# Optimization experiments

Hardware: AMD Instinct MI355X
Metric: run time of the kernel (lower is better)

The kernel has to match this reference:

```python
import jax, jax.numpy as jnp
import numpy as np

N_NODES = 10000
N_EDGES = 160000
H = 128          # n_hidden_feat
K1 = 64          # n_Gaussian
K2 = 64          # n_grid_K**3
NB = 3           # N_block
G = 100          # number of graphs in batch
CUTOFF = 8.0


def setup_inputs() -> dict:
    key = jax.random.key(0)
    ks = jax.random.split(key, 20)
    s = 0.05
    return {
        'x': jax.random.normal(ks[0], (N_NODES, H), jnp.float32),
        'edge_distance': jax.random.uniform(ks[1], (N_EDGES,), jnp.float32, 0.5, 10.0),
        'combine_sets': jax.random.normal(ks[2], (N_EDGES, K1), jnp.float32),
        'plane_wave': jax.random.normal(ks[3], (N_EDGES, K2), jnp.float32),
        'emb_W': jax.random.normal(ks[4], (H, H), jnp.float32) * s,
        'conv_Wgate': jax.random.normal(ks[5], (NB, 3 * H, H), jnp.float32) * s,
        'conv_Wmlp': jax.random.normal(ks[6], (NB, 3 * H, H), jnp.float32) * s,
        'conv_W1': jax.random.normal(ks[7], (NB, K1, H), jnp.float32) * s,
        'conv_W2g': jax.random.normal(ks[8], (NB, K2, K2), jnp.float32) * s,
        'conv_W2': jax.random.normal(ks[9], (NB, K2, H), jnp.float32) * s,
        'pool_W1': jax.random.normal(ks[10], (NB, H, H), jnp.float32) * s,
        'pool_W2': jax.random.normal(ks[11], (NB, H, H), jnp.float32) * s,
        'psi_W': jax.random.normal(ks[12], (NB, H, H), jnp.float32) * s,
        'lr_W1': jax.random.normal(ks[13], (H, H // 2), jnp.float32) * s,
        'lr_W2': jax.random.normal(ks[14], (H // 2, H // 4), jnp.float32) * s,
        'edge_sources': jax.random.randint(ks[15], (N_EDGES,), 0, N_NODES, jnp.int32),
        'edge_targets': jax.random.randint(ks[16], (N_EDGES,), 0, N_NODES, jnp.int32),
        'graph_indices': jnp.sort(jax.random.randint(ks[17], (N_NODES,), 0, G, jnp.int32)),
        'node_counts': jax.random.randint(ks[18], (G,), 1, 200, jnp.int32),
    }


def reference(x, edge_distance, combine_sets, plane_wave, emb_W,
              conv_Wgate, conv_Wmlp, conv_W1, conv_W2g, conv_W2,
              pool_W1, pool_W2, psi_W, lr_W1, lr_W2,
              edge_sources, edge_targets, graph_indices, node_counts):
    n_graphs = node_counts.shape[0]
    elu = jax.nn.elu
    sig = jax.nn.sigmoid

    # NodeEmbedding (sigmoid activation, no bias)
    h = sig(x @ emb_W)                                   # [N, H]

    r = edge_distance[:, None]                           # [E, 1]
    mask = (r < CUTOFF).astype(h.dtype)                  # [E, 1]

    pooled_sum = jnp.zeros((n_graphs, h.shape[1]), h.dtype)
    for i in range(conv_Wgate.shape[0]):                 # N_block (small fixed)
        # --- GatedGraphConvolution ---
        ni = h[edge_sources]                             # [E, H] gather
        nj = h[edge_targets]                             # [E, H] gather
        fe = jnp.concatenate([ni, nj, (ni - nj) / r], axis=1)  # [E, 3H]
        e_gate = sig(fe @ conv_Wgate[i])                 # [E, H]
        e_mlp = elu(fe @ conv_Wmlp[i])                   # [E, H]
        z1 = combine_sets @ conv_W1[i]                   # [E, H]
        pw_gate = sig(plane_wave @ conv_W2g[i])          # [E, K2]
        z2 = (plane_wave * pw_gate) @ conv_W2[i]         # [E, H]
        z = e_gate * e_mlp * (z1 + z2) * mask            # [E, H]
        h = h.at[edge_sources].add(z)                    # scatter-add (index_add_)
        # --- Gated_pooling (note: original discards /node_counts -> sum pool) ---
        zp = elu((h @ pool_W1[i]) * (h @ pool_W2[i]))    # [N, H]
        pooled_sum = pooled_sum + jax.ops.segment_sum(zp, graph_indices, num_segments=n_graphs)
        # --- MLP_psi2n ---
        h = elu(h @ psi_W[i])

    y = elu(pooled_sum @ lr_W1)                          # [G, H/2]
    y = elu(y @ lr_W2)                                   # [G, H/4]
    return y
```

## Files before the change

### kernel.cpp

```cpp
#include <hip/hip_runtime.h>
#include <math.h>

#define H 128
#define N_NODES 10000
#define N_EDGES 160000

typedef float f32x4 __attribute__((ext_vector_type(4)));
typedef short s16x8 __attribute__((ext_vector_type(8)));

#define WAVE_LDS_FENCE() do { \
  asm volatile("s_waitcnt lgkmcnt(0)" ::: "memory"); \
  __builtin_amdgcn_sched_barrier(0); \
} while (0)

__device__ __forceinline__ float sigf(float x){ return 1.0f/(1.0f + __expf(-x)); }
__device__ __forceinline__ float eluf(float x){ return x > 0.0f ? x : (__expf(x) - 1.0f); }

__device__ __forceinline__ unsigned short f2bf(float f){
  unsigned int u = __float_as_uint(f);
  unsigned int r = (u + 0x7fffu + ((u >> 16) & 1u)) >> 16;
  return (unsigned short)r;
}
__device__ __forceinline__ float bf2f(unsigned short s){
  return __uint_as_float(((unsigned int)s) << 16);
}

__device__ __forceinline__ f32x4 MFMA16(s16x8 a, s16x8 b, f32x4 c){
  return __builtin_amdgcn_mfma_f32_16x16x32_bf16(a, b, c, 0, 0, 0);
}

__device__ __forceinline__ s16x8 loadA_f32(const float* p){
  float4 a = *(const float4*)p;
  float4 b = *(const float4*)(p+4);
  s16x8 r;
  r[0]=(short)f2bf(a.x); r[1]=(short)f2bf(a.y); r[2]=(short)f2bf(a.z); r[3]=(short)f2bf(a.w);
  r[4]=(short)f2bf(b.x); r[5]=(short)f2bf(b.y); r[6]=(short)f2bf(b.z); r[7]=(short)f2bf(b.w);
  return r;
}

__global__ __launch_bounds__(256) void hist_kernel(
    const int* __restrict__ src, const float* __restrict__ ed, int* __restrict__ count)
{
  int e = blockIdx.x*256 + threadIdx.x;
  if (e < N_EDGES && ed[e] < 8.0f) atomicAdd(&count[src[e]], 1);
}

__global__ __launch_bounds__(256) void scan_kernel(
    const int* __restrict__ count, int* __restrict__ offsets)
{
  __shared__ int tmp[256];
  __shared__ int sbase;
  if (threadIdx.x == 0) sbase = 0;
  __syncthreads();
  for (int c0 = 0; c0 < N_NODES; c0 += 256) {
    int i = c0 + threadIdx.x;
    int v = (i < N_NODES) ? count[i] : 0;
    tmp[threadIdx.x] = v;
    __syncthreads();
    for (int off = 1; off < 256; off <<= 1) {
      int t = (threadIdx.x >= off) ? tmp[threadIdx.x - off] : 0;
      __syncthreads();
      tmp[threadIdx.x] += t;
      __syncthreads();
    }
    if (i < N_NODES) offsets[i] = sbase + tmp[threadIdx.x] - v;
    __syncthreads();
    if (threadIdx.x == 255) sbase += tmp[255];
    __syncthreads();
  }
  if (threadIdx.x == 0) offsets[N_NODES] = sbase;
}

__global__ __launch_bounds__(256) void scatter_kernel(
    const int* __restrict__ src, const int* __restrict__ tgt, const float* __restrict__ ed,
    const int* __restrict__ offsets,
    int* __restrict__ cursor, int* __restrict__ mcur, int* __restrict__ perm,
    int* __restrict__ srcp, int* __restrict__ tgtp, float* __restrict__ edp)
{
  int e = blockIdx.x*256 + threadIdx.x;
  if (e < N_EDGES) {
    int s = src[e];
    float r = ed[e];
    int pos;
    if (r < 8.0f) pos = atomicAdd(&cursor[s], 1);
    else          pos = offsets[N_NODES] + atomicAdd(mcur, 1);
    perm[pos] = e;
    srcp[pos] = s;
    tgtp[pos] = tgt[e];
    edp[pos]  = r;
  }
}

__global__ __launch_bounds__(256) void prep_edges(
    const float* __restrict__ cs, const float* __restrict__ pw, const int* __restrict__ perm,
    unsigned short* __restrict__ csb, unsigned short* __restrict__ pwb)
{
  int idx = blockIdx.x*256 + threadIdx.x;
  if (idx >= N_EDGES*8) return;
  int pos = idx >> 3, kc = idx & 7;
  int e = perm[pos];
  s16x8 c = loadA_f32(&cs[(size_t)e*64 + kc*8]);
  s16x8 p = loadA_f32(&pw[(size_t)e*64 + kc*8]);
  *(s16x8*)&csb[(size_t)pos*64 + kc*8] = c;
  *(s16x8*)&pwb[(size_t)pos*64 + kc*8] = p;
}

__global__ __launch_bounds__(256) void prep_weights(
    const float* __restrict__ W1, const float* __restrict__ W2, const float* __restrict__ W2g,
    const float* __restrict__ embW,
    unsigned short* __restrict__ w1t, unsigned short* __restrict__ w2t,
    unsigned short* __restrict__ w2gt, unsigned short* __restrict__ embt)
{
  int idx = blockIdx.x*256 + threadIdx.x;
  if (idx < 3*8192) {
    int l = idx / 8192, r = idx % 8192;
    int c = r >> 6, k = r & 63;
    w1t[idx] = f2bf(W1[l*8192 + k*128 + c]);
    w2t[idx] = f2bf(W2[l*8192 + k*128 + c]);
  } else if (idx < 3*8192 + 3*4096) {
    int idx2 = idx - 3*8192;
    int l = idx2 / 4096, r = idx2 % 4096;
    int c = r >> 6, k = r & 63;
    w2gt[idx2] = f2bf(W2g[l*4096 + k*64 + c]);
  } else {
    int idx3 = idx - (3*8192 + 3*4096);
    if (idx3 < 16384) {
      int c = idx3 >> 7, k = idx3 & 127;
      embt[idx3] = f2bf(embW[k*128 + c]);
    }
  }
}

__global__ __launch_bounds__(256) void prep_nodew(
    const float* __restrict__ Wg, const float* __restrict__ Wm,
    const float* __restrict__ p1, const float* __restrict__ p2, const float* __restrict__ psiW,
    unsigned short* __restrict__ wnt, unsigned short* __restrict__ wpt)
{
  int idx = blockIdx.x*256 + threadIdx.x;
  if (idx < 3*98304) {
    int l = idx / 98304, r = idx % 98304;
    int j = r >> 7, k = r & 127;
    float v;
    if (j < 384) v = Wg[l*49152 + (j>>7)*16384 + k*128 + (j&127)];
    else { int jj = j - 384; v = Wm[l*49152 + (jj>>7)*16384 + k*128 + (jj&127)]; }
    wnt[idx] = f2bf(v);
  } else {
    int idx2 = idx - 3*98304;
    if (idx2 < 3*49152) {
      int l = idx2 / 49152, r = idx2 % 49152;
      int j = r >> 7, k = r & 127;
      float v;
      if (j < 128)      v = p1 [l*16384 + k*128 + j];
      else if (j < 256) v = p2 [l*16384 + k*128 + (j-128)];
      else              v = psiW[l*16384 + k*128 + (j-256)];
      wpt[idx2] = f2bf(v);
    }
  }
}

__global__ __launch_bounds__(256) void embed_pack(
    const float* __restrict__ x, const unsigned short* __restrict__ embt,
    const unsigned short* __restrict__ wnt,
    float* __restrict__ h_out,
    unsigned short* __restrict__ spackb, unsigned short* __restrict__ tpackb)
{
  __shared__ unsigned short hb[16*128];
  int tid = threadIdx.x, wave = tid >> 6, lane = tid & 63;
  int row = lane & 15, kg = lane >> 4;
  int nbase = blockIdx.x*16;
  const float* xr = &x[(size_t)(nbase + row)*H];
  s16x8 a[4];
  #pragma unroll
  for (int ks = 0; ks < 4; ks++) a[ks] = loadA_f32(xr + ks*32 + kg*8);

  f32x4 acc[2];
  #pragma unroll
  for (int ti = 0; ti < 2; ti++) { acc[ti][0]=0.f; acc[ti][1]=0.f; acc[ti][2]=0.f; acc[ti][3]=0.f; }
  #pragma unroll
  for (int ti = 0; ti < 2; ti++) {
    int col = (wave*2 + ti)*16 + row;
    #pragma unroll
    for (int ks = 0; ks < 4; ks++) {
      s16x8 b = *(const s16x8*)&embt[(size_t)col*128 + ks*32 + kg*8];
      acc[ti] = MFMA16(a[ks], b, acc[ti]);
    }
  }
  #pragma unroll
  for (int ti = 0; ti < 2; ti++) {
    int col = (wave*2 + ti)*16 + row;
    #pragma unroll
    for (int r = 0; r < 4; r++) {
      int ln = kg*4 + r;
      float v = sigf(acc[ti][r]);
      h_out[(size_t)(nbase + ln)*H + col] = v;
      int byt = (ln << 8) + (col << 1);
      byt ^= (ln & 7) << 4;
      *(unsigned short*)((char*)hb + byt) = f2bf(v);
    }
  }
  __syncthreads();

  s16x8 an[4];
  #pragma unroll
  for (int ks = 0; ks < 4; ks++) {
    int byt = (row << 8) + ks*64 + kg*16;
    byt ^= (row & 7) << 4;
    an[ks] = *(s16x8*)((char*)hb + byt);
  }
  #pragma unroll
  for (int ti = 0; ti < 2; ti++) {
    int t = wave*2 + ti;
    f32x4 pacc[6];
    #pragma unroll
    for (int ch = 0; ch < 6; ch++) { pacc[ch][0]=0.f; pacc[ch][1]=0.f; pacc[ch][2]=0.f; pacc[ch][3]=0.f; }
    #pragma unroll
    for (int ch = 0; ch < 6; ch++) {
      int col = ch*128 + t*16 + row;
      #pragma unroll
      for (int ks = 0; ks < 4; ks++) {
        s16x8 b = *(const s16x8*)&wnt[(size_t)col*128 + ks*32 + kg*8];
        pacc[ch] = MFMA16(an[ks], b, pacc[ch]);
      }
    }
    int c = t*16 + row;
    #pragma unroll
    for (int r = 0; r < 4; r++) {
      int nc = nbase + kg*4 + r;
      size_t base = (size_t)nc*512 + c*4;
      unsigned int s0 = (unsigned int)f2bf(pacc[0][r]) | ((unsigned int)f2bf(pacc[2][r]) << 16);
      unsigned int s1 = (unsigned int)f2bf(pacc[3][r]) | ((unsigned int)f2bf(pacc[5][r]) << 16);
      unsigned int t0 = (unsigned int)f2bf(pacc[1][r]) | ((unsigned int)f2bf(pacc[2][r]) << 16);
      unsigned int t1 = (unsigned int)f2bf(pacc[4][r]) | ((unsigned int)f2bf(pacc[5][r]) << 16);
      *(uint2*)&spackb[base] = make_uint2(s0, s1);
      *(uint2*)&tpackb[base] = make_uint2(t0, t1);
    }
  }
}

__global__ __launch_bounds__(256) void fused_edge(
    float* __restrict__ h_acc,
    const unsigned short* __restrict__ csb, const unsigned short* __restrict__ pwb,
    const unsigned short* __restrict__ w1t, const unsigned short* __restrict__ w2t,
    const unsigned short* __restrict__ w2gt,
    const int* __restrict__ srcp, const int* __restrict__ tgtp,
    const float* __restrict__ edp, const int* __restrict__ nact,
    const unsigned short* __restrict__ spackb, const unsigned short* __restrict__ tpackb)
{
  __shared__ unsigned short zb[4][16][132];
  __shared__ int   src_s[4][16];
  __shared__ int   tgt_s[4][16];
  __shared__ float rcp_s[4][16];
  __shared__ float msk_s[4][16];

  int p0 = blockIdx.x * 64;
  if (p0 >= *nact) return;

  int tid  = threadIdx.x;
  int wave = tid >> 6, lane = tid & 63;
  int row  = lane & 15, kg = lane >> 4;
  unsigned short* gate = &zb[wave][0][0];

  if (lane < 16) {
    int e = p0 + wave*16 + lane;
    float r = edp[e];
    rcp_s[wave][lane] = 1.0f / r;
    msk_s[wave][lane] = (r < 8.0f) ? 1.0f : 0.0f;
    src_s[wave][lane] = srcp[e];
    tgt_s[wave][lane] = tgtp[e];
  }

  int pos = p0 + wave*16 + row;
  s16x8 acs[2], apw[2];
  acs[0] = *(const s16x8*)&csb[(size_t)pos*64 + kg*8];
  acs[1] = *(const s16x8*)&csb[(size_t)pos*64 + 32 + kg*8];
  apw[0] = *(const s16x8*)&pwb[(size_t)pos*64 + kg*8];
  apw[1] = *(const s16x8*)&pwb[(size_t)pos*64 + 32 + kg*8];

  f32x4 acc1[4];
  #pragma unroll
  for (int nt = 0; nt < 4; nt++) { acc1[nt][0]=0.f; acc1[nt][1]=0.f; acc1[nt][2]=0.f; acc1[nt][3]=0.f; }
  #pragma unroll
  for (int nt = 0; nt < 4; nt++) {
    s16x8 b0 = *(const s16x8*)&w2gt[(size_t)(nt*16+row)*64 + kg*8];
    s16x8 b1 = *(const s16x8*)&w2gt[(size_t)(nt*16+row)*64 + 32 + kg*8];
    acc1[nt] = MFMA16(apw[0], b0, acc1[nt]);
    acc1[nt] = MFMA16(apw[1], b1, acc1[nt]);
  }

  #pragma unroll
  for (int nt = 0; nt < 4; nt++) {
    #pragma unroll
    for (int r = 0; r < 4; r++) {
      int grow = kg*4 + r;
      int gcol = nt*16 + row;
      int byt = (grow << 7) + (gcol << 1);
      byt ^= (grow & 7) << 4;
      *(unsigned short*)((char*)gate + byt) = f2bf(sigf(acc1[nt][r]));
    }
  }
  WAVE_LDS_FENCE();

  s16x8 apg[2];
  #pragma unroll
  for (int ks = 0; ks < 2; ks++) {
    int byt = (row << 7) + ks*64 + kg*16;
    byt ^= (row & 7) << 4;
    s16x8 g = *(s16x8*)((char*)gate + byt);
    s16x8 o;
    #pragma unroll
    for (int j = 0; j < 8; j++) {
      float v = bf2f((unsigned short)apw[ks][j]) * bf2f((unsigned short)g[j]);
      o[j] = (short)f2bf(v);
    }
    apg[ks] = o;
  }
  WAVE_LDS_FENCE();

  f32x4 acc2[8];
  #pragma unroll
  for (int nt = 0; nt < 8; nt++) { acc2[nt][0]=0.f; acc2[nt][1]=0.f; acc2[nt][2]=0.f; acc2[nt][3]=0.f; }
  #pragma unroll
  for (int nt = 0; nt < 8; nt++) {
    #pragma unroll
    for (int ks = 0; ks < 2; ks++) {
      s16x8 b1 = *(const s16x8*)&w1t[(size_t)(nt*16+row)*64 + ks*32 + kg*8];
      acc2[nt] = MFMA16(acs[ks], b1, acc2[nt]);
      s16x8 b2 = *(const s16x8*)&w2t[(size_t)(nt*16+row)*64 + ks*32 + kg*8];
      acc2[nt] = MFMA16(apg[ks], b2, acc2[nt]);
    }
  }

  #pragma unroll
  for (int nt = 0; nt < 8; nt++) {
    #pragma unroll
    for (int r = 0; r < 4; r++) {
      zb[wave][kg*4 + r][nt*16 + row] = f2bf(acc2[nt][r]);
    }
  }
  WAVE_LDS_FENCE();

  {
    int l = lane;
    int cur = src_s[wave][0];
    s16x8 sp = *(const s16x8*)&spackb[(size_t)cur*512 + l*8];
    float Ags0 = bf2f((unsigned short)sp[0]), Cgs0 = bf2f((unsigned short)sp[1]);
    float Ams0 = bf2f((unsigned short)sp[2]), Cms0 = bf2f((unsigned short)sp[3]);
    float Ags1 = bf2f((unsigned short)sp[4]), Cgs1 = bf2f((unsigned short)sp[5]);
    float Ams1 = bf2f((unsigned short)sp[6]), Cms1 = bf2f((unsigned short)sp[7]);
    float acc0 = 0.f, accB = 0.f;
    for (int eb = 0; eb < 16; eb += 4) {
      s16x8 tp[4]; unsigned int zz[4];
      #pragma unroll
      for (int b = 0; b < 4; b++) {
        int e = eb + b;
        tp[b] = *(const s16x8*)&tpackb[(size_t)tgt_s[wave][e]*512 + l*8];
        zz[b] = *(const unsigned int*)&zb[wave][e][2*l];
      }
      #pragma unroll
      for (int b = 0; b < 4; b++) {
        int e = eb + b;
        int sn = src_s[wave][e];
        if (sn != cur) {
          atomicAdd(&h_acc[(size_t)cur*H + 2*l],     acc0);
          atomicAdd(&h_acc[(size_t)cur*H + 2*l + 1], accB);
          acc0 = 0.f; accB = 0.f; cur = sn;
          sp = *(const s16x8*)&spackb[(size_t)cur*512 + l*8];
          Ags0 = bf2f((unsigned short)sp[0]); Cgs0 = bf2f((unsigned short)sp[1]);
          Ams0 = bf2f((unsigned short)sp[2]); Cms0 = bf2f((unsigned short)sp[3]);
          Ags1 = bf2f((unsigned short)sp[4]); Cgs1 = bf2f((unsigned short)sp[5]);
          Ams1 = bf2f((unsigned short)sp[6]); Cms1 = bf2f((unsigned short)sp[7]);
        }
        float rc = rcp_s[wave][e], mk = msk_s[wave][e];
        float z0 = bf2f((unsigned short)(zz[b] & 0xffffu));
        float z1 = bf2f((unsigned short)(zz[b] >> 16));
        float Bg0 = bf2f((unsigned short)tp[b][0]), Cg0 = bf2f((unsigned short)tp[b][1]);
        float Bm0 = bf2f((unsigned short)tp[b][2]), Cm0 = bf2f((unsigned short)tp[b][3]);
        float Bg1 = bf2f((unsigned short)tp[b][4]), Cg1 = bf2f((unsigned short)tp[b][5]);
        float Bm1 = bf2f((unsigned short)tp[b][6]), Cm1 = bf2f((unsigned short)tp[b][7]);
        float g0 = sigf(Ags0 + Bg0 + rc*(Cgs0 - Cg0));
        float m0 = eluf(Ams0 + Bm0 + rc*(Cms0 - Cm0));
        acc0 += g0 * m0 * z0 * mk;
        float g1 = sigf(Ags1 + Bg1 + rc*(Cgs1 - Cg1));
        float m1 = eluf(Ams1 + Bm1 + rc*(Cms1 - Cm1));
        accB += g1 * m1 * z1 * mk;
      }
    }
    atomicAdd(&h_acc[(size_t)cur*H + 2*l],     acc0);
    atomicAdd(&h_acc[(size_t)cur*H + 2*l + 1], accB);
  }
}

__global__ __launch_bounds__(256) void node_next(
    float* __restrict__ h,
    const unsigned short* __restrict__ wpt,
    const unsigned short* __restrict__ wnt,
    const int* __restrict__ gidx, float* __restrict__ pooled,
    unsigned short* __restrict__ spackb, unsigned short* __restrict__ tpackb,
    int has_next)
{
  __shared__ unsigned short hb[16*128];
  int tid = threadIdx.x, wave = tid >> 6, lane = tid & 63;
  int row = lane & 15, kg = lane >> 4;
  int nbase = blockIdx.x*16;
  const float* hr = &h[(size_t)(nbase + row)*H];
  s16x8 a[4];
  #pragma unroll
  for (int ks = 0; ks < 4; ks++) a[ks] = loadA_f32(hr + ks*32 + kg*8);

  f32x4 acc1[2], acc2[2], acc3[2];
  #pragma unroll
  for (int ti = 0; ti < 2; ti++) {
    #pragma unroll
    for (int r = 0; r < 4; r++) { acc1[ti][r]=0.f; acc2[ti][r]=0.f; acc3[ti][r]=0.f; }
  }
  #pragma unroll
  for (int ti = 0; ti < 2; ti++) {
    int col = (wave*2 + ti)*16 + row;
    #pragma unroll
    for (int ks = 0; ks < 4; ks++) {
      s16x8 b1 = *(const s16x8*)&wpt[(size_t)(col      )*128 + ks*32 + kg*8];
      s16x8 b2 = *(const s16x8*)&wpt[(size_t)(col + 128)*128 + ks*32 + kg*8];
      s16x8 b3 = *(const s16x8*)&wpt[(size_t)(col + 256)*128 + ks*32 + kg*8];
      acc1[ti] = MFMA16(a[ks], b1, acc1[ti]);
      acc2[ti] = MFMA16(a[ks], b2, acc2[ti]);
      acc3[ti] = MFMA16(a[ks], b3, acc3[ti]);
    }
  }

  int nc0 = nbase + kg*4;
  int g0 = gidx[nc0], g3 = gidx[nc0 + 3];
  if (g0 == g3) {
    #pragma unroll
    for (int ti = 0; ti < 2; ti++) {
      int col = (wave*2 + ti)*16 + row;
      float s = 0.f;
      #pragma unroll
      for (int r = 0; r < 4; r++) s += eluf(acc1[ti][r] * acc2[ti][r]);
      atomicAdd(&pooled[g0*H + col], s);
      #pragma unroll
      for (int r = 0; r < 4; r++) {
        int ln = kg*4 + r;
        float v = eluf(acc3[ti][r]);
        h[(size_t)(nc0 + r)*H + col] = v;
        int byt = (ln << 8) + (col << 1);
        byt ^= (ln & 7) << 4;
        *(unsigned short*)((char*)hb + byt) = f2bf(v);
      }
    }
  } else {
    #pragma unroll
    for (int r = 0; r < 4; r++) {
      int nc = nc0 + r;
      int ln = kg*4 + r;
      int g = gidx[nc];
      #pragma unroll
      for (int ti = 0; ti < 2; ti++) {
        int col = (wave*2 + ti)*16 + row;
        float zp = eluf(acc1[ti][r] * acc2[ti][r]);
        atomicAdd(&pooled[g*H + col], zp);
        float v = eluf(acc3[ti][r]);
        h[(size_t)nc*H + col] = v;
        int byt = (ln << 8) + (col << 1);
        byt ^= (ln & 7) << 4;
        *(unsigned short*)((char*)hb + byt) = f2bf(v);
      }
    }
  }
  if (!has_next) return;
  __syncthreads();

  s16x8 an[4];
  #pragma unroll
  for (int ks = 0; ks < 4; ks++) {
    int byt = (row << 8) + ks*64 + kg*16;
    byt ^= (row & 7) << 4;
    an[ks] = *(s16x8*)((char*)hb + byt);
  }
  #pragma unroll
  for (int ti = 0; ti < 2; ti++) {
    int t = wave*2 + ti;
    f32x4 pacc[6];
    #pragma unroll
    for (int ch = 0; ch < 6; ch++) { pacc[ch][0]=0.f; pacc[ch][1]=0.f; pacc[ch][2]=0.f; pacc[ch][3]=0.f; }
    #pragma unroll
    for (int ch = 0; ch < 6; ch++) {
      int col = ch*128 + t*16 + row;
      #pragma unroll
      for (int ks = 0; ks < 4; ks++) {
        s16x8 b = *(const s16x8*)&wnt[(size_t)col*128 + ks*32 + kg*8];
        pacc[ch] = MFMA16(an[ks], b, pacc[ch]);
      }
    }
    int c = t*16 + row;
    #pragma unroll
    for (int r = 0; r < 4; r++) {
      int nc = nbase + kg*4 + r;
      size_t base = (size_t)nc*512 + c*4;
      unsigned int s0 = (unsigned int)f2bf(pacc[0][r]) | ((unsigned int)f2bf(pacc[2][r]) << 16);
      unsigned int s1 = (unsigned int)f2bf(pacc[3][r]) | ((unsigned int)f2bf(pacc[5][r]) << 16);
      unsigned int t0 = (unsigned int)f2bf(pacc[1][r]) | ((unsigned int)f2bf(pacc[2][r]) << 16);
      unsigned int t1 = (unsigned int)f2bf(pacc[4][r]) | ((unsigned int)f2bf(pacc[5][r]) << 16);
      *(uint2*)&spackb[base] = make_uint2(s0, s1);
      *(uint2*)&tpackb[base] = make_uint2(t0, t1);
    }
  }
}

__global__ __launch_bounds__(64) void final_kernel(
    const float* __restrict__ pooled, const float* __restrict__ lr1, const float* __restrict__ lr2,
    float* __restrict__ out)
{
  __shared__ float sp[128];
  __shared__ float y1[64];
  int g = blockIdx.x, tid = threadIdx.x;
  sp[tid]      = pooled[g*128 + tid];
  sp[tid + 64] = pooled[g*128 + 64 + tid];
  __syncthreads();
  float acc = 0.f;
  for (int k = 0; k < 128; k++) acc += sp[k] * lr1[k*64 + tid];
  y1[tid] = eluf(acc);
  __syncthreads();
  if (tid < 32) {
    float a2 = 0.f;
    for (int k = 0; k < 64; k++) a2 += y1[k] * lr2[k*32 + tid];
    out[g*32 + tid] = eluf(a2);
  }
}

extern "C" void kernel_launch(void* const* d_in, const int* in_sizes, int n_in,
                              void* d_out, int out_size, void* d_ws, size_t ws_size,
                              hipStream_t stream)
{
  const float* x    = (const float*)d_in[0];
  const float* ed   = (const float*)d_in[1];
  const float* cs   = (const float*)d_in[2];
  const float* pw   = (const float*)d_in[3];
  const float* embW = (const float*)d_in[4];
  const float* Wg   = (const float*)d_in[5];
  const float* Wm   = (const float*)d_in[6];
  const float* W1   = (const float*)d_in[7];
  const float* W2g  = (const float*)d_in[8];
  const float* W2   = (const float*)d_in[9];
  const float* p1   = (const float*)d_in[10];
  const float* p2   = (const float*)d_in[11];
  const float* psiW = (const float*)d_in[12];
  const float* lr1  = (const float*)d_in[13];
  const float* lr2  = (const float*)d_in[14];
  const int* esrc   = (const int*)d_in[15];
  const int* etgt   = (const int*)d_in[16];
  const int* gidx   = (const int*)d_in[17];

  float* h_b    = (float*)d_ws;
  float* pooled = h_b + (size_t)N_NODES*H;
  unsigned short* spackb = (unsigned short*)(pooled + 100*H);
  unsigned short* tpackb = spackb + (size_t)N_NODES*512;
  int* counts  = (int*)(tpackb + (size_t)N_NODES*512);
  int* offsets = counts + N_NODES;
  int* cursor  = offsets + N_NODES + 1;
  int* mcur    = cursor + N_NODES;
  int* perm    = mcur + 1;
  int* srcp    = perm + N_EDGES;
  int* tgtp    = srcp + N_EDGES;
  float* edp   = (float*)(tgtp + N_EDGES);
  unsigned short* w1t  = (unsigned short*)(edp + N_EDGES);
  unsigned short* w2t  = w1t + 3*8192;
  unsigned short* w2gt = w2t + 3*8192;
  unsigned short* embt = w2gt + 3*4096;
  unsigned short* wnt  = embt + 16384;
  unsigned short* wpt  = wnt + 3*98304;
  unsigned short* csb  = wpt + 3*49152;
  unsigned short* pwb  = csb + (size_t)N_EDGES*64;

  hipMemsetAsync(counts, 0, N_NODES*sizeof(int), stream);
  hipMemsetAsync(mcur, 0, sizeof(int), stream);
  hipMemsetAsync(pooled, 0, 100*H*sizeof(float), stream);
  hist_kernel<<<(N_EDGES+255)/256, 256, 0, stream>>>(esrc, ed, counts);
  scan_kernel<<<1, 256, 0, stream>>>(counts, offsets);
  hipMemcpyAsync(cursor, offsets, N_NODES*sizeof(int), hipMemcpyDeviceToDevice, stream);
  scatter_kernel<<<(N_EDGES+255)/256, 256, 0, stream>>>(esrc, etgt, ed, offsets,
      cursor, mcur, perm, srcp, tgtp, edp);
  prep_edges<<<N_EDGES*8/256, 256, 0, stream>>>(cs, pw, perm, csb, pwb);
  prep_weights<<<208, 256, 0, stream>>>(W1, W2, W2g, embW, w1t, w2t, w2gt, embt);
  prep_nodew<<<(3*98304 + 3*49152 + 255)/256, 256, 0, stream>>>(Wg, Wm, p1, p2, psiW, wnt, wpt);

  embed_pack<<<N_NODES/16, 256, 0, stream>>>(x, embt, wnt, h_b, spackb, tpackb);

  for (int i = 0; i < 3; i++) {
    fused_edge<<<N_EDGES/64, 256, 0, stream>>>(h_b, csb, pwb,
        w1t + i*8192, w2t + i*8192, w2gt + i*4096,
        srcp, tgtp, edp, offsets + N_NODES, spackb, tpackb);
    node_next<<<N_NODES/16, 256, 0, stream>>>(h_b,
        wpt + i*49152, wnt + ((i+1) % 3)*98304,
        gidx, pooled, spackb, tpackb, (i < 2) ? 1 : 0);
  }
  final_kernel<<<100, 64, 0, stream>>>(pooled, lr1, lr2, (float*)d_out);
}
```

Measured before the change: 428.6 us.

## Process 32 edges per wave in fused_edge and widen node_next to 8 waves

fused_edge now handles 128 edges per block, with each wave doing two 16-row sub-tiles, which halves the grid and lengthens each wave's scatter run so fewer atomic flushes happen at segment boundaries. node_next runs with 512 threads, one 16-column tile per wave instead of two, to raise parallelism and cut per-thread register use. prep_edges zero-fills rows past the active edge count and skips their gathers, so the now-padded tiles read defined data and no work is spent on masked edges. The costs are higher LDS and register use per fused_edge block and an extra block-wide barrier in node_next.

Result: slower. 461.4 us (+7.7%).

```diff
diff --git a/kernel.cpp b/kernel.cpp
--- a/kernel.cpp
+++ b/kernel.cpp
@@ -93,16 +93,23 @@
 
 __global__ __launch_bounds__(256) void prep_edges(
     const float* __restrict__ cs, const float* __restrict__ pw, const int* __restrict__ perm,
+    const int* __restrict__ nact,
     unsigned short* __restrict__ csb, unsigned short* __restrict__ pwb)
 {
   int idx = blockIdx.x*256 + threadIdx.x;
   if (idx >= N_EDGES*8) return;
   int pos = idx >> 3, kc = idx & 7;
-  int e = perm[pos];
-  s16x8 c = loadA_f32(&cs[(size_t)e*64 + kc*8]);
-  s16x8 p = loadA_f32(&pw[(size_t)e*64 + kc*8]);
-  *(s16x8*)&csb[(size_t)pos*64 + kc*8] = c;
-  *(s16x8*)&pwb[(size_t)pos*64 + kc*8] = p;
+  if (pos < *nact) {
+    int e = perm[pos];
+    s16x8 c = loadA_f32(&cs[(size_t)e*64 + kc*8]);
+    s16x8 p = loadA_f32(&pw[(size_t)e*64 + kc*8]);
+    *(s16x8*)&csb[(size_t)pos*64 + kc*8] = c;
+    *(s16x8*)&pwb[(size_t)pos*64 + kc*8] = p;
+  } else {
+    s16x8 z = {0,0,0,0,0,0,0,0};
+    *(s16x8*)&csb[(size_t)pos*64 + kc*8] = z;
+    *(s16x8*)&pwb[(size_t)pos*64 + kc*8] = z;
+  }
 }
 
 __global__ __launch_bounds__(256) void prep_weights(
@@ -246,22 +253,21 @@
     const float* __restrict__ edp, const int* __restrict__ nact,
     const unsigned short* __restrict__ spackb, const unsigned short* __restrict__ tpackb)
 {
-  __shared__ unsigned short zb[4][16][132];
-  __shared__ int   src_s[4][16];
-  __shared__ int   tgt_s[4][16];
-  __shared__ float rcp_s[4][16];
-  __shared__ float msk_s[4][16];
-
-  int p0 = blockIdx.x * 64;
+  __shared__ unsigned short zb[4][32][132];
+  __shared__ int   src_s[4][32];
+  __shared__ int   tgt_s[4][32];
+  __shared__ float rcp_s[4][32];
+  __shared__ float msk_s[4][32];
+
+  int p0 = blockIdx.x * 128;
   if (p0 >= *nact) return;
 
   int tid  = threadIdx.x;
   int wave = tid >> 6, lane = tid & 63;
   int row  = lane & 15, kg = lane >> 4;
-  unsigned short* gate = &zb[wave][0][0];
-
-  if (lane < 16) {
-    int e = p0 + wave*16 + lane;
+
+  if (lane < 32) {
+    int e = p0 + wave*32 + lane;
     float r = edp[e];
     rcp_s[wave][lane] = 1.0f / r;
     msk_s[wave][lane] = (r < 8.0f) ? 1.0f : 0.0f;
@@ -269,72 +275,76 @@
     tgt_s[wave][lane] = tgtp[e];
   }
 
-  int pos = p0 + wave*16 + row;
-  s16x8 acs[2], apw[2];
-  acs[0] = *(const s16x8*)&csb[(size_t)pos*64 + kg*8];
-  acs[1] = *(const s16x8*)&csb[(size_t)pos*64 + 32 + kg*8];
-  apw[0] = *(const s16x8*)&pwb[(size_t)pos*64 + kg*8];
-  apw[1] = *(const s16x8*)&pwb[(size_t)pos*64 + 32 + kg*8];
-
-  f32x4 acc1[4];
-  #pragma unroll
-  for (int nt = 0; nt < 4; nt++) { acc1[nt][0]=0.f; acc1[nt][1]=0.f; acc1[nt][2]=0.f; acc1[nt][3]=0.f; }
-  #pragma unroll
-  for (int nt = 0; nt < 4; nt++) {
-    s16x8 b0 = *(const s16x8*)&w2gt[(size_t)(nt*16+row)*64 + kg*8];
-    s16x8 b1 = *(const s16x8*)&w2gt[(size_t)(nt*16+row)*64 + 32 + kg*8];
-    acc1[nt] = MFMA16(apw[0], b0, acc1[nt]);
-    acc1[nt] = MFMA16(apw[1], b1, acc1[nt]);
-  }
-
-  #pragma unroll
-  for (int nt = 0; nt < 4; nt++) {
-    #pragma unroll
-    for (int r = 0; r < 4; r++) {
-      int grow = kg*4 + r;
-      int gcol = nt*16 + row;
-      int byt = (grow << 7) + (gcol << 1);
-      byt ^= (grow & 7) << 4;
-      *(unsigned short*)((char*)gate + byt) = f2bf(sigf(acc1[nt][r]));
-    }
-  }
-  WAVE_LDS_FENCE();
-
-  s16x8 apg[2];
-  #pragma unroll
-  for (int ks = 0; ks < 2; ks++) {
-    int byt = (row << 7) + ks*64 + kg*16;
-    byt ^= (row & 7) << 4;
-    s16x8 g = *(s16x8*)((char*)gate + byt);
-    s16x8 o;
-    #pragma unroll
-    for (int j = 0; j < 8; j++) {
-      float v = bf2f((unsigned short)apw[ks][j]) * bf2f((unsigned short)g[j]);
-      o[j] = (short)f2bf(v);
-    }
-    apg[ks] = o;
-  }
-  WAVE_LDS_FENCE();
-
-  f32x4 acc2[8];
-  #pragma unroll
-  for (int nt = 0; nt < 8; nt++) { acc2[nt][0]=0.f; acc2[nt][1]=0.f; acc2[nt][2]=0.f; acc2[nt][3]=0.f; }
-  #pragma unroll
-  for (int nt = 0; nt < 8; nt++) {
+  #pragma unroll
+  for (int hf2 = 0; hf2 < 2; hf2++) {
+    unsigned short* gate = &zb[wave][hf2*16][0];
+    int pos = p0 + wave*32 + hf2*16 + row;
+    s16x8 acs[2], apw[2];
+    acs[0] = *(const s16x8*)&csb[(size_t)pos*64 + kg*8];
+    acs[1] = *(const s16x8*)&csb[(size_t)pos*64 + 32 + kg*8];
+    apw[0] = *(const s16x8*)&pwb[(size_t)pos*64 + kg*8];
+    apw[1] = *(const s16x8*)&pwb[(size_t)pos*64 + 32 + kg*8];
+
+    f32x4 acc1[4];
+    #pragma unroll
+    for (int nt = 0; nt < 4; nt++) { acc1[nt][0]=0.f; acc1[nt][1]=0.f; acc1[nt][2]=0.f; acc1[nt][3]=0.f; }
+    #pragma unroll
+    for (int nt = 0; nt < 4; nt++) {
+      s16x8 b0 = *(const s16x8*)&w2gt[(size_t)(nt*16+row)*64 + kg*8];
+      s16x8 b1 = *(const s16x8*)&w2gt[(size_t)(nt*16+row)*64 + 32 + kg*8];
+      acc1[nt] = MFMA16(apw[0], b0, acc1[nt]);
+      acc1[nt] = MFMA16(apw[1], b1, acc1[nt]);
+    }
+
+    #pragma unroll
+    for (int nt = 0; nt < 4; nt++) {
+      #pragma unroll
+      for (int r = 0; r < 4; r++) {
+        int grow = kg*4 + r;
+        int gcol = nt*16 + row;
+        int byt = (grow << 7) + (gcol << 1);
+        byt ^= (grow & 7) << 4;
+        *(unsigned short*)((char*)gate + byt) = f2bf(sigf(acc1[nt][r]));
+      }
+    }
+    WAVE_LDS_FENCE();
+
+    s16x8 apg[2];
     #pragma unroll
     for (int ks = 0; ks < 2; ks++) {
-      s16x8 b1 = *(const s16x8*)&w1t[(size_t)(nt*16+row)*64 + ks*32 + kg*8];
-      acc2[nt] = MFMA16(acs[ks], b1, acc2[nt]);
-      s16x8 b2 = *(const s16x8*)&w2t[(size_t)(nt*16+row)*64 + ks*32 + kg*8];
-      acc2[nt] = MFMA16(apg[ks], b2, acc2[nt]);
-    }
-  }
-
-  #pragma unroll
-  for (int nt = 0; nt < 8; nt++) {
-    #pragma unroll
-    for (int r = 0; r < 4; r++) {
-      zb[wave][kg*4 + r][nt*16 + row] = f2bf(acc2[nt][r]);
+      int byt = (row << 7) + ks*64 + kg*16;
+      byt ^= (row & 7) << 4;
+      s16x8 g = *(s16x8*)((char*)gate + byt);
+      s16x8 o;
+      #pragma unroll
+      for (int j = 0; j < 8; j++) {
+        float v = bf2f((unsigned short)apw[ks][j]) * bf2f((unsigned short)g[j]);
+        o[j] = (short)f2bf(v);
+      }
+      apg[ks] = o;
+    }
+    WAVE_LDS_FENCE();
+
+    f32x4 acc2[8];
+    #pragma unroll
+    for (int nt = 0; nt < 8; nt++) { acc2[nt][0]=0.f; acc2[nt][1]=0.f; acc2[nt][2]=0.f; acc2[nt][3]=0.f; }
+    #pragma unroll
+    for (int nt = 0; nt < 8; nt++) {
+      #pragma unroll
+      for (int ks = 0; ks < 2; ks++) {
+        s16x8 b1 = *(const s16x8*)&w1t[(size_t)(nt*16+row)*64 + ks*32 + kg*8];
+        acc2[nt] = MFMA16(acs[ks], b1, acc2[nt]);
+        s16x8 b2 = *(const s16x8*)&w2t[(size_t)(nt*16+row)*64 + ks*32 + kg*8];
+        acc2[nt] = MFMA16(apg[ks], b2, acc2[nt]);
+      }
+    }
+
+    #pragma unroll
+    for (int nt = 0; nt < 8; nt++) {
+      #pragma unroll
+      for (int r = 0; r < 4; r++) {
+        zb[wave][hf2*16 + kg*4 + r][nt*16 + row] = f2bf(acc2[nt][r]);
+      }
     }
   }
   WAVE_LDS_FENCE();
@@ -348,7 +358,7 @@
     float Ags1 = bf2f((unsigned short)sp[4]), Cgs1 = bf2f((unsigned short)sp[5]);
     float Ams1 = bf2f((unsigned short)sp[6]), Cms1 = bf2f((unsigned short)sp[7]);
     float acc0 = 0.f, accB = 0.f;
-    for (int eb = 0; eb < 16; eb += 4) {
+    for (int eb = 0; eb < 32; eb += 4) {
       s16x8 tp[4]; unsigned int zz[4];
       #pragma unroll
       for (int b = 0; b < 4; b++) {
@@ -390,7 +400,7 @@
   }
 }
 
-__global__ __launch_bounds__(256) void node_next(
+__global__ __launch_bounds__(512) void node_next(
     float* __restrict__ h,
     const unsigned short* __restrict__ wpt,
     const unsigned short* __restrict__ wnt,
@@ -406,46 +416,37 @@
   s16x8 a[4];
   #pragma unroll
   for (int ks = 0; ks < 4; ks++) a[ks] = loadA_f32(hr + ks*32 + kg*8);
-
-  f32x4 acc1[2], acc2[2], acc3[2];
-  #pragma unroll
-  for (int ti = 0; ti < 2; ti++) {
-    #pragma unroll
-    for (int r = 0; r < 4; r++) { acc1[ti][r]=0.f; acc2[ti][r]=0.f; acc3[ti][r]=0.f; }
-  }
-  #pragma unroll
-  for (int ti = 0; ti < 2; ti++) {
-    int col = (wave*2 + ti)*16 + row;
-    #pragma unroll
-    for (int ks = 0; ks < 4; ks++) {
-      s16x8 b1 = *(const s16x8*)&wpt[(size_t)(col      )*128 + ks*32 + kg*8];
-      s16x8 b2 = *(const s16x8*)&wpt[(size_t)(col + 128)*128 + ks*32 + kg*8];
-      s16x8 b3 = *(const s16x8*)&wpt[(size_t)(col + 256)*128 + ks*32 + kg*8];
-      acc1[ti] = MFMA16(a[ks], b1, acc1[ti]);
-      acc2[ti] = MFMA16(a[ks], b2, acc2[ti]);
-      acc3[ti] = MFMA16(a[ks], b3, acc3[ti]);
-    }
+  __syncthreads();
+
+  int col = wave*16 + row;
+  f32x4 acc1, acc2, acc3;
+  acc1[0]=0.f; acc1[1]=0.f; acc1[2]=0.f; acc1[3]=0.f;
+  acc2 = acc1; acc3 = acc1;
+  #pragma unroll
+  for (int ks = 0; ks < 4; ks++) {
+    s16x8 b1 = *(const s16x8*)&wpt[(size_t)(col      )*128 + ks*32 + kg*8];
+    s16x8 b2 = *(const s16x8*)&wpt[(size_t)(col + 128)*128 + ks*32 + kg*8];
+    s16x8 b3 = *(const s16x8*)&wpt[(size_t)(col + 256)*128 + ks*32 + kg*8];
+    acc1 = MFMA16(a[ks], b1, acc1);
+    acc2 = MFMA16(a[ks], b2, acc2);
+    acc3 = MFMA16(a[ks], b3, acc3);
   }
 
   int nc0 = nbase + kg*4;
   int g0 = gidx[nc0], g3 = gidx[nc0 + 3];
   if (g0 == g3) {
-    #pragma unroll
-    for (int ti = 0; ti < 2; ti++) {
-      int col = (wave*2 + ti)*16 + row;
-      float s = 0.f;
-      #pragma unroll
-      for (int r = 0; r < 4; r++) s += eluf(acc1[ti][r] * acc2[ti][r]);
-      atomicAdd(&pooled[g0*H + col], s);
-      #pragma unroll
-      for (int r = 0; r < 4; r++) {
-        int ln = kg*4 + r;
-        float v = eluf(acc3[ti][r]);
-        h[(size_t)(nc0 + r)*H + col] = v;
-        int byt = (ln << 8) + (col << 1);
-        byt ^= (ln & 7) << 4;
-        *(unsigned short*)((char*)hb + byt) = f2bf(v);
-      }
+    float s = 0.f;
+    #pragma unroll
+    for (int r = 0; r < 4; r++) s += eluf(acc1[r] * acc2[r]);
+    atomicAdd(&pooled[g0*H + col], s);
+    #pragma unroll
+    for (int r = 0; r < 4; r++) {
+      int ln = kg*4 + r;
+      float v = eluf(acc3[r]);
+      h[(size_t)(nc0 + r)*H + col] = v;
+      int byt = (ln << 8) + (col << 1);
+      byt ^= (ln & 7) << 4;
+      *(unsigned short*)((char*)hb + byt) = f2bf(v);
     }
   } else {
     #pragma unroll
@@ -453,17 +454,13 @@
       int nc = nc0 + r;
       int ln = kg*4 + r;
       int g = gidx[nc];
-      #pragma unroll
-      for (int ti = 0; ti < 2; ti++) {
-        int col = (wave*2 + ti)*16 + row;
-        float zp = eluf(acc1[ti][r] * acc2[ti][r]);
-        atomicAdd(&pooled[g*H + col], zp);
-        float v = eluf(acc3[ti][r]);
-        h[(size_t)nc*H + col] = v;
-        int byt = (ln << 8) + (col << 1);
-        byt ^= (ln & 7) << 4;
-        *(unsigned short*)((char*)hb + byt) = f2bf(v);
-      }
+      float zp = eluf(acc1[r] * acc2[r]);
+      atomicAdd(&pooled[g*H + col], zp);
+      float v = eluf(acc3[r]);
+      h[(size_t)nc*H + col] = v;
+      int byt = (ln << 8) + (col << 1);
+      byt ^= (ln & 7) << 4;
+      *(unsigned short*)((char*)hb + byt) = f2bf(v);
     }
   }
   if (!has_next) return;
@@ -476,33 +473,29 @@
     byt ^= (row & 7) << 4;
     an[ks] = *(s16x8*)((char*)hb + byt);
   }
-  #pragma unroll
-  for (int ti = 0; ti < 2; ti++) {
-    int t = wave*2 + ti;
-    f32x4 pacc[6];
-    #pragma unroll
-    for (int ch = 0; ch < 6; ch++) { pacc[ch][0]=0.f; pacc[ch][1]=0.f; pacc[ch][2]=0.f; pacc[ch][3]=0.f; }
-    #pragma unroll
-    for (int ch = 0; ch < 6; ch++) {
-      int col = ch*128 + t*16 + row;
-      #pragma unroll
-      for (int ks = 0; ks < 4; ks++) {
-        s16x8 b = *(const s16x8*)&wnt[(size_t)col*128 + ks*32 + kg*8];
-        pacc[ch] = MFMA16(an[ks], b, pacc[ch]);
-      }
-    }
-    int c = t*16 + row;
-    #pragma unroll
-    for (int r = 0; r < 4; r++) {
-      int nc = nbase + kg*4 + r;
-      size_t base = (size_t)nc*512 + c*4;
-      unsigned int s0 = (unsigned int)f2bf(pacc[0][r]) | ((unsigned int)f2bf(pacc[2][r]) << 16);
-      unsigned int s1 = (unsigned int)f2bf(pacc[3][r]) | ((unsigned int)f2bf(pacc[5][r]) << 16);
-      unsigned int t0 = (unsigned int)f2bf(pacc[1][r]) | ((unsigned int)f2bf(pacc[2][r]) << 16);
-      unsigned int t1 = (unsigned int)f2bf(pacc[4][r]) | ((unsigned int)f2bf(pacc[5][r]) << 16);
-      *(uint2*)&spackb[base] = make_uint2(s0, s1);
-      *(uint2*)&tpackb[base] = make_uint2(t0, t1);
-    }
+  f32x4 pacc[6];
+  #pragma unroll
+  for (int ch = 0; ch < 6; ch++) { pacc[ch][0]=0.f; pacc[ch][1]=0.f; pacc[ch][2]=0.f; pacc[ch][3]=0.f; }
+  #pragma unroll
+  for (int ch = 0; ch < 6; ch++) {
+    int pcol = ch*128 + wave*16 + row;
+    #pragma unroll
+    for (int ks = 0; ks < 4; ks++) {
+      s16x8 b = *(const s16x8*)&wnt[(size_t)pcol*128 + ks*32 + kg*8];
+      pacc[ch] = MFMA16(an[ks], b, pacc[ch]);
+    }
+  }
+  int c = wave*16 + row;
+  #pragma unroll
+  for (int r = 0; r < 4; r++) {
+    int nc = nbase + kg*4 + r;
+    size_t base = (size_t)nc*512 + c*4;
+    unsigned int s0 = (unsigned int)f2bf(pacc[0][r]) | ((unsigned int)f2bf(pacc[2][r]) << 16);
+    unsigned int s1 = (unsigned int)f2bf(pacc[3][r]) | ((unsigned int)f2bf(pacc[5][r]) << 16);
+    unsigned int t0 = (unsigned int)f2bf(pacc[1][r]) | ((unsigned int)f2bf(pacc[2][r]) << 16);
+    unsigned int t1 = (unsigned int)f2bf(pacc[4][r]) | ((unsigned int)f2bf(pacc[5][r]) << 16);
+    *(uint2*)&spackb[base] = make_uint2(s0, s1);
+    *(uint2*)&tpackb[base] = make_uint2(t0, t1);
   }
 }
 
@@ -579,17 +572,17 @@
   hipMemcpyAsync(cursor, offsets, N_NODES*sizeof(int), hipMemcpyDeviceToDevice, stream);
   scatter_kernel<<<(N_EDGES+255)/256, 256, 0, stream>>>(esrc, etgt, ed, offsets,
       cursor, mcur, perm, srcp, tgtp, edp);
-  prep_edges<<<N_EDGES*8/256, 256, 0, stream>>>(cs, pw, perm, csb, pwb);
+  prep_edges<<<N_EDGES*8/256, 256, 0, stream>>>(cs, pw, perm, offsets + N_NODES, csb, pwb);
   prep_weights<<<208, 256, 0, stream>>>(W1, W2, W2g, embW, w1t, w2t, w2gt, embt);
   prep_nodew<<<(3*98304 + 3*49152 + 255)/256, 256, 0, stream>>>(Wg, Wm, p1, p2, psiW, wnt, wpt);
 
   embed_pack<<<N_NODES/16, 256, 0, stream>>>(x, embt, wnt, h_b, spackb, tpackb);
 
   for (int i = 0; i < 3; i++) {
-    fused_edge<<<N_EDGES/64, 256, 0, stream>>>(h_b, csb, pwb,
+    fused_edge<<<N_EDGES/128, 256, 0, stream>>>(h_b, csb, pwb,
         w1t + i*8192, w2t + i*8192, w2gt + i*4096,
         srcp, tgtp, edp, offsets + N_NODES, spackb, tpackb);
-    node_next<<<N_NODES/16, 256, 0, stream>>>(h_b,
+    node_next<<<N_NODES/16, 512, 0, stream>>>(h_b,
         wpt + i*49152, wnt + ((i+1) % 3)*98304,
         gidx, pooled, spackb, tpackb, (i < 2) ? 1 : 0);
   }
```
